# Optimization experiments

Measured on AMD Instinct MI355X. Metric: run time of the kernel, lower is better.

## Reference

```python
import jax, jax.numpy as jnp
import numpy as np

N, K, D = 524288, 32, 8
EPS = 1e-6


def setup_inputs() -> dict:
    key = jax.random.key(0)
    k1, k2, k3, k4 = jax.random.split(key, 4)
    x = jax.random.normal(k1, (N, D), dtype=jnp.float32)
    pi = jax.random.uniform(k2, (K,), dtype=jnp.float32)
    means = jax.random.normal(k3, (K, D), dtype=jnp.float32)
    # eye + small perturbation keeps tril(chol_var) well-conditioned (PD covariance)
    chol_var = jnp.eye(D, dtype=jnp.float32)[None] + 0.1 * jax.random.normal(k4, (K, D, D), dtype=jnp.float32)
    return {"x": x, "pi": pi, "means": means, "chol_var": chol_var}


def reference(x, pi, means, chol_var):
    d = x.shape[-1]
    L = jnp.tril(chol_var)                                   # [K,d,d]
    cov = jnp.einsum('kij,klj->kil', L, L) + EPS * jnp.eye(d, dtype=x.dtype)
    C = jnp.linalg.cholesky(cov)                             # [K,d,d] (MVN recomputes cholesky)
    logdet = 2.0 * jnp.sum(jnp.log(jnp.diagonal(C, axis1=-2, axis2=-1)), axis=-1)  # [K]
    eye = jnp.eye(d, dtype=x.dtype)
    Cinv = jax.vmap(lambda c: jax.scipy.linalg.solve_triangular(c, eye, lower=True))(C)  # [K,d,d]
    zx = jnp.einsum('kij,nj->nki', Cinv, x)                  # [N,K,d]
    zm = jnp.einsum('kij,kj->ki', Cinv, means)               # [K,d]
    maha = jnp.sum((zx - zm[None]) ** 2, axis=-1)            # [N,K]
    log_2pi = jnp.log(2.0 * jnp.pi).astype(x.dtype)
    log_probs = -0.5 * (maha + d * log_2pi + logdet[None])   # [N,K]
    wll = log_probs + jax.nn.log_softmax(pi)[None]
    return jax.scipy.special.logsumexp(wll, axis=1)          # [N]
```

## Files before the change

kernel.cpp:

```cpp
#include <hip/hip_runtime.h>
#include <math.h>

#define K_ 32
#define D_ 8
#define NF 48
#define NTHREADS 256
#define NBLOCKS 1024
#define TPW 4

typedef _Float16 half8 __attribute__((ext_vector_type(8)));
typedef float f32x16 __attribute__((ext_vector_type(16)));

__global__ __launch_bounds__(NTHREADS) void gmm_mfma(
    const float* __restrict__ x,
    const float* __restrict__ pi,
    const float* __restrict__ means,
    const float* __restrict__ chol,
    float* __restrict__ out, int N)
{
    __shared__ __align__(16) _Float16 ldsA[3][64][8];

    const int tid = threadIdx.x;

    if (tid < K_) {
        const int k = tid;
        float L[D_][D_];
#pragma unroll
        for (int i = 0; i < D_; ++i)
#pragma unroll
            for (int j = 0; j <= i; ++j)
                L[i][j] = chol[k * 64 + i * 8 + j];

        float rd[D_];
#pragma unroll
        for (int i = 0; i < D_; ++i) rd[i] = 1.f / L[i][i];

        float Ci[D_][D_];
#pragma unroll
        for (int j = 0; j < D_; ++j) {
            Ci[j][j] = rd[j];
#pragma unroll
            for (int i = j + 1; i < D_; ++i) {
                float s = 0.f;
#pragma unroll
                for (int m = j; m < i; ++m) s += L[i][m] * Ci[m][j];
                Ci[i][j] = -s * rd[i];
            }
        }

        float logdet = 0.f;
#pragma unroll
        for (int i = 0; i < D_; ++i) logdet += __logf(fabsf(L[i][i]));
        logdet *= 2.f;

        float A2[D_][D_];
#pragma unroll
        for (int i = 0; i < D_; ++i)
#pragma unroll
            for (int j = 0; j <= i; ++j) {
                float s = 0.f;
#pragma unroll
                for (int m = i; m < D_; ++m) s += Ci[m][i] * Ci[m][j];
                A2[i][j] = s;
                A2[j][i] = s;
            }

        float mu[D_];
#pragma unroll
        for (int j = 0; j < D_; ++j) mu[j] = means[k * 8 + j];
        float b[D_], q = 0.f;
#pragma unroll
        for (int i = 0; i < D_; ++i) {
            float s = 0.f;
#pragma unroll
            for (int j = 0; j < D_; ++j) s += A2[i][j] * mu[j];
            b[i] = s;
            q += s * mu[i];
        }

        float mx = pi[0];
#pragma unroll
        for (int t = 1; t < K_; ++t) mx = fmaxf(mx, pi[t]);
        float se = 0.f;
#pragma unroll
        for (int t = 0; t < K_; ++t) se += __expf(pi[t] - mx);
        float lse = mx + __logf(se);

        const float LOG2PI = 1.8378770664093453f;
        const float LOG2E  = 1.4426950408889634f;
        const float ALPHA  = 0.72134752044448170f;
        float cst2 = ((pi[k] - lse) - 0.5f * (logdet + 8.f * LOG2PI)) * LOG2E;

        float V[NF];
        int t = 0;
#pragma unroll
        for (int i = 0; i < D_; ++i)
#pragma unroll
            for (int j = 0; j <= i; ++j)
                V[t++] = (i == j) ? -ALPHA * A2[i][i] : -2.f * ALPHA * A2[i][j];
#pragma unroll
        for (int i = 0; i < D_; ++i) V[36 + i] = 2.f * ALPHA * b[i];
        V[44] = cst2 - ALPHA * q;
        V[45] = 0.f; V[46] = 0.f; V[47] = 0.f;

#pragma unroll
        for (int s = 0; s < 3; ++s)
#pragma unroll
            for (int h = 0; h < 2; ++h)
#pragma unroll
                for (int j = 0; j < 8; ++j)
                    ldsA[s][h * 32 + k][j] = (_Float16)V[16 * s + 8 * h + j];
    }
    __syncthreads();

    const int lane = tid & 63;
    const int m    = lane & 31;
    const bool h1  = lane >= 32;

    half8 wf[3];
#pragma unroll
    for (int s = 0; s < 3; ++s) wf[s] = *(const half8*)&ldsA[s][lane][0];

    const int w  = blockIdx.x * (NTHREADS / 64) + (tid >> 6);
    const int t0 = w * TPW;
    const float4* xp = (const float4*)x;
    const float LN2 = 0.69314718055994531f;

    float xv[TPW][D_];
#pragma unroll
    for (int u = 0; u < TPW; ++u) {
        const int n = (t0 + u) * 32 + m;
        float4 a = xp[2 * n], b2 = xp[2 * n + 1];
        xv[u][0] = a.x;  xv[u][1] = a.y;  xv[u][2] = a.z;  xv[u][3] = a.w;
        xv[u][4] = b2.x; xv[u][5] = b2.y; xv[u][6] = b2.z; xv[u][7] = b2.w;
    }

#pragma unroll
    for (int u = 0; u < TPW; ++u) {
        float Y[NF];
        {
            int t = 0;
#pragma unroll
            for (int i = 0; i < D_; ++i)
#pragma unroll
                for (int j = 0; j <= i; ++j) Y[t++] = xv[u][i] * xv[u][j];
#pragma unroll
            for (int i = 0; i < D_; ++i) Y[36 + i] = xv[u][i];
            Y[44] = 1.f; Y[45] = 0.f; Y[46] = 0.f; Y[47] = 0.f;
        }

        f32x16 acc;
#pragma unroll
        for (int r = 0; r < 16; ++r) acc[r] = 0.f;

#pragma unroll
        for (int s = 0; s < 3; ++s) {
            half8 bf;
#pragma unroll
            for (int j = 0; j < 8; ++j) {
                float v = h1 ? Y[16 * s + 8 + j] : Y[16 * s + j];
                bf[j] = (_Float16)v;
            }
            acc = __builtin_amdgcn_mfma_f32_32x32x16_f16(wf[s], bf, acc, 0, 0, 0);
        }

        float tot = 0.f;
#pragma unroll
        for (int r = 0; r < 16; ++r) tot += exp2f(acc[r]);
        tot += __shfl_xor(tot, 32, 64);
        float res = log2f(tot) * LN2;
        if (!h1) out[(t0 + u) * 32 + m] = res;
    }
}

extern "C" void kernel_launch(void* const* d_in, const int* in_sizes, int n_in,
                              void* d_out, int out_size, void* d_ws, size_t ws_size,
                              hipStream_t stream) {
    const float* x     = (const float*)d_in[0];
    const float* pi    = (const float*)d_in[1];
    const float* means = (const float*)d_in[2];
    const float* chol  = (const float*)d_in[3];
    float* out = (float*)d_out;

    int N = in_sizes[0] / D_;

    gmm_mfma<<<NBLOCKS, NTHREADS, 0, stream>>>(x, pi, means, chol, out, N);
}
```

Measured before the change: 75.06 us.

## Split per-component parameter prep into separate kernel via workspace

Moves the per-component Cholesky inverse and quadratic-form coefficient computation out of every block into a single-block prep kernel. That kernel writes the fp16 MFMA A-operand to workspace, and the main kernel loads it from global memory, so the LDS buffer and __syncthreads go away. This removes the redundant prep work that all 1024 blocks used to serialize on before any MFMA work. The feature vector is also built per MFMA slice instead of as one full array, and launch bounds ask for 4 blocks per CU. The cost is a second kernel launch and its dependency, with a single-thread-per-component prep stage on the critical path.

After: 109.2 us. +45.5%, slower.

```diff
diff --git a/kernel.cpp b/kernel.cpp
--- a/kernel.cpp
+++ b/kernel.cpp
@@ -11,115 +11,113 @@
 typedef _Float16 half8 __attribute__((ext_vector_type(8)));
 typedef float f32x16 __attribute__((ext_vector_type(16)));
 
-__global__ __launch_bounds__(NTHREADS) void gmm_mfma(
-    const float* __restrict__ x,
+
+__global__ void gmm_prep(
     const float* __restrict__ pi,
     const float* __restrict__ means,
     const float* __restrict__ chol,
-    float* __restrict__ out, int N)
+    _Float16* __restrict__ wsV)
 {
-    __shared__ __align__(16) _Float16 ldsA[3][64][8];
+    const int k = threadIdx.x;
+    if (k >= K_) return;
 
-    const int tid = threadIdx.x;
+    float L[D_][D_];
+#pragma unroll
+    for (int i = 0; i < D_; ++i)
+#pragma unroll
+        for (int j = 0; j <= i; ++j)
+            L[i][j] = chol[k * 64 + i * 8 + j];
 
-    if (tid < K_) {
-        const int k = tid;
-        float L[D_][D_];
+    float rd[D_];
 #pragma unroll
-        for (int i = 0; i < D_; ++i)
+    for (int i = 0; i < D_; ++i) rd[i] = 1.f / L[i][i];
+
+    float Ci[D_][D_];
 #pragma unroll
-            for (int j = 0; j <= i; ++j)
-                L[i][j] = chol[k * 64 + i * 8 + j];
+    for (int j = 0; j < D_; ++j) {
+        Ci[j][j] = rd[j];
+#pragma unroll
+        for (int i = j + 1; i < D_; ++i) {
+            float s = 0.f;
+#pragma unroll
+            for (int m = j; m < i; ++m) s += L[i][m] * Ci[m][j];
+            Ci[i][j] = -s * rd[i];
+        }
+    }
 
-        float rd[D_];
+    float logdet = 0.f;
 #pragma unroll
-        for (int i = 0; i < D_; ++i) rd[i] = 1.f / L[i][i];
+    for (int i = 0; i < D_; ++i) logdet += __logf(fabsf(L[i][i]));
+    logdet *= 2.f;
 
-        float Ci[D_][D_];
+    float A2[D_][D_];
 #pragma unroll
-        for (int j = 0; j < D_; ++j) {
-            Ci[j][j] = rd[j];
+    for (int i = 0; i < D_; ++i)
 #pragma unroll
-            for (int i = j + 1; i < D_; ++i) {
-                float s = 0.f;
+        for (int j = 0; j <= i; ++j) {
+            float s = 0.f;
 #pragma unroll
-                for (int m = j; m < i; ++m) s += L[i][m] * Ci[m][j];
-                Ci[i][j] = -s * rd[i];
-            }
+            for (int m = i; m < D_; ++m) s += Ci[m][i] * Ci[m][j];
+            A2[i][j] = s;
+            A2[j][i] = s;
         }
 
-        float logdet = 0.f;
+    float mu[D_];
 #pragma unroll
-        for (int i = 0; i < D_; ++i) logdet += __logf(fabsf(L[i][i]));
-        logdet *= 2.f;
+    for (int j = 0; j < D_; ++j) mu[j] = means[k * 8 + j];
+    float b[D_], q = 0.f;
+#pragma unroll
+    for (int i = 0; i < D_; ++i) {
+        float s = 0.f;
+#pragma unroll
+        for (int j = 0; j < D_; ++j) s += A2[i][j] * mu[j];
+        b[i] = s;
+        q += s * mu[i];
+    }
 
-        float A2[D_][D_];
+    float mx = pi[0];
 #pragma unroll
-        for (int i = 0; i < D_; ++i)
+    for (int t = 1; t < K_; ++t) mx = fmaxf(mx, pi[t]);
+    float se = 0.f;
 #pragma unroll
-            for (int j = 0; j <= i; ++j) {
-                float s = 0.f;
+    for (int t = 0; t < K_; ++t) se += __expf(pi[t] - mx);
+    float lse = mx + __logf(se);
+
+    const float LOG2PI = 1.8378770664093453f;
+    const float LOG2E  = 1.4426950408889634f;
+    const float ALPHA  = 0.72134752044448170f;
+    float cst2 = ((pi[k] - lse) - 0.5f * (logdet + 8.f * LOG2PI)) * LOG2E;
+
+    float V[NF];
+    int t = 0;
 #pragma unroll
-                for (int m = i; m < D_; ++m) s += Ci[m][i] * Ci[m][j];
-                A2[i][j] = s;
-                A2[j][i] = s;
-            }
-
-        float mu[D_];
+    for (int i = 0; i < D_; ++i)
 #pragma unroll
-        for (int j = 0; j < D_; ++j) mu[j] = means[k * 8 + j];
-        float b[D_], q = 0.f;
+        for (int j = 0; j <= i; ++j)
+            V[t++] = (i == j) ? -ALPHA * A2[i][i] : -2.f * ALPHA * A2[i][j];
 #pragma unroll
-        for (int i = 0; i < D_; ++i) {
-            float s = 0.f;
-#pragma unroll
-            for (int j = 0; j < D_; ++j) s += A2[i][j] * mu[j];
-            b[i] = s;
-            q += s * mu[i];
-        }
-
-        float mx = pi[0];
-#pragma unroll
-        for (int t = 1; t < K_; ++t) mx = fmaxf(mx, pi[t]);
-        float se = 0.f;
-#pragma unroll
-        for (int t = 0; t < K_; ++t) se += __expf(pi[t] - mx);
-        float lse = mx + __logf(se);
-
-        const float LOG2PI = 1.8378770664093453f;
-        const float LOG2E  = 1.4426950408889634f;
-        const float ALPHA  = 0.72134752044448170f;
-        float cst2 = ((pi[k] - lse) - 0.5f * (logdet + 8.f * LOG2PI)) * LOG2E;
-
-        float V[NF];
-        int t = 0;
-#pragma unroll
-        for (int i = 0; i < D_; ++i)
-#pragma unroll
-            for (int j = 0; j <= i; ++j)
-                V[t++] = (i == j) ? -ALPHA * A2[i][i] : -2.f * ALPHA * A2[i][j];
-#pragma unroll
-        for (int i = 0; i < D_; ++i) V[36 + i] = 2.f * ALPHA * b[i];
-        V[44] = cst2 - ALPHA * q;
-        V[45] = 0.f; V[46] = 0.f; V[47] = 0.f;
+    for (int i = 0; i < D_; ++i) V[36 + i] = 2.f * ALPHA * b[i];
+    V[44] = cst2 - ALPHA * q;
+    V[45] = 0.f; V[46] = 0.f; V[47] = 0.f;
 
 #pragma unroll
-        for (int s = 0; s < 3; ++s)
+    for (int s = 0; s < 3; ++s)
 #pragma unroll
-            for (int h = 0; h < 2; ++h)
+        for (int h = 0; h < 2; ++h)
 #pragma unroll
-                for (int j = 0; j < 8; ++j)
-                    ldsA[s][h * 32 + k][j] = (_Float16)V[16 * s + 8 * h + j];
-    }
-    __syncthreads();
+            for (int j = 0; j < 8; ++j)
+                wsV[(s * 64 + h * 32 + k) * 8 + j] = (_Float16)V[16 * s + 8 * h + j];
+}
 
+__global__ __launch_bounds__(NTHREADS, 4) void gmm_mfma(
+    const float* __restrict__ x,
+    const _Float16* __restrict__ wsV,
+    float* __restrict__ out)
+{
+    const int tid  = threadIdx.x;
     const int lane = tid & 63;
     const int m    = lane & 31;
     const bool h1  = lane >= 32;
-
-    half8 wf[3];
-#pragma unroll
-    for (int s = 0; s < 3; ++s) wf[s] = *(const half8*)&ldsA[s][lane][0];
 
     const int w  = blockIdx.x * (NTHREADS / 64) + (tid >> 6);
     const int t0 = w * TPW;
@@ -135,30 +133,40 @@
         xv[u][4] = b2.x; xv[u][5] = b2.y; xv[u][6] = b2.z; xv[u][7] = b2.w;
     }
 
+    const half8* wp = (const half8*)wsV;
+    half8 wf[3];
+#pragma unroll
+    for (int s = 0; s < 3; ++s) wf[s] = wp[s * 64 + lane];
+
 #pragma unroll
     for (int u = 0; u < TPW; ++u) {
-        float Y[NF];
-        {
-            int t = 0;
-#pragma unroll
-            for (int i = 0; i < D_; ++i)
-#pragma unroll
-                for (int j = 0; j <= i; ++j) Y[t++] = xv[u][i] * xv[u][j];
-#pragma unroll
-            for (int i = 0; i < D_; ++i) Y[36 + i] = xv[u][i];
-            Y[44] = 1.f; Y[45] = 0.f; Y[46] = 0.f; Y[47] = 0.f;
-        }
-
         f32x16 acc;
 #pragma unroll
         for (int r = 0; r < 16; ++r) acc[r] = 0.f;
 
 #pragma unroll
         for (int s = 0; s < 3; ++s) {
+            float yb[16];
+            int t = 0;
+#pragma unroll
+            for (int i = 0; i < D_; ++i)
+#pragma unroll
+                for (int j = 0; j <= i; ++j) {
+                    if (t >= 16 * s && t < 16 * (s + 1))
+                        yb[t - 16 * s] = xv[u][i] * xv[u][j];
+                    ++t;
+                }
+#pragma unroll
+            for (int i = 0; i < D_; ++i) {
+                const int f = 36 + i;
+                if (f >= 16 * s && f < 16 * (s + 1)) yb[f - 16 * s] = xv[u][i];
+            }
+            if (s == 2) { yb[12] = 1.f; yb[13] = 0.f; yb[14] = 0.f; yb[15] = 0.f; }
+
             half8 bf;
 #pragma unroll
             for (int j = 0; j < 8; ++j) {
-                float v = h1 ? Y[16 * s + 8 + j] : Y[16 * s + j];
+                float v = h1 ? yb[8 + j] : yb[j];
                 bf[j] = (_Float16)v;
             }
             acc = __builtin_amdgcn_mfma_f32_32x32x16_f16(wf[s], bf, acc, 0, 0, 0);
@@ -181,8 +189,9 @@
     const float* means = (const float*)d_in[2];
     const float* chol  = (const float*)d_in[3];
     float* out = (float*)d_out;
+    _Float16* wsV = (_Float16*)d_ws;
+    (void)in_sizes; (void)n_in; (void)out_size; (void)ws_size;
 
-    int N = in_sizes[0] / D_;
-
-    gmm_mfma<<<NBLOCKS, NTHREADS, 0, stream>>>(x, pi, means, chol, out, N);
+    gmm_prep<<<1, 64, 0, stream>>>(pi, means, chol, wsV);
+    gmm_mfma<<<NBLOCKS, NTHREADS, 0, stream>>>(x, wsV, out);
 }
```

## Compute per-component weights in every lane, dropping LDS and block barrier

Applied to the files above, without the earlier changes.

Each lane now does the Cholesky inverse and quadratic-form coefficient setup for its own component (k = lane%32) directly in registers. This replaces the old scheme where 32 threads per block computed them, wrote them to LDS, and the block synchronized. The kernel also issues half of the x loads before this setup so memory latency overlaps with it, vectorizes the parameter loads, and adds a launch-bounds occupancy hint. The cost is redundant setup math in every lane and higher register pressure.

Result: slower. 136.8 us (+82.3%).

```diff
diff --git a/kernel.cpp b/kernel.cpp
--- a/kernel.cpp
+++ b/kernel.cpp
@@ -11,115 +11,18 @@
 typedef _Float16 half8 __attribute__((ext_vector_type(8)));
 typedef float f32x16 __attribute__((ext_vector_type(16)));
 
-__global__ __launch_bounds__(NTHREADS) void gmm_mfma(
+__global__ __launch_bounds__(NTHREADS, 4) void gmm_mfma(
     const float* __restrict__ x,
     const float* __restrict__ pi,
     const float* __restrict__ means,
     const float* __restrict__ chol,
-    float* __restrict__ out, int N)
+    float* __restrict__ out)
 {
-    __shared__ __align__(16) _Float16 ldsA[3][64][8];
-
-    const int tid = threadIdx.x;
-
-    if (tid < K_) {
-        const int k = tid;
-        float L[D_][D_];
-#pragma unroll
-        for (int i = 0; i < D_; ++i)
-#pragma unroll
-            for (int j = 0; j <= i; ++j)
-                L[i][j] = chol[k * 64 + i * 8 + j];
-
-        float rd[D_];
-#pragma unroll
-        for (int i = 0; i < D_; ++i) rd[i] = 1.f / L[i][i];
-
-        float Ci[D_][D_];
-#pragma unroll
-        for (int j = 0; j < D_; ++j) {
-            Ci[j][j] = rd[j];
-#pragma unroll
-            for (int i = j + 1; i < D_; ++i) {
-                float s = 0.f;
-#pragma unroll
-                for (int m = j; m < i; ++m) s += L[i][m] * Ci[m][j];
-                Ci[i][j] = -s * rd[i];
-            }
-        }
-
-        float logdet = 0.f;
-#pragma unroll
-        for (int i = 0; i < D_; ++i) logdet += __logf(fabsf(L[i][i]));
-        logdet *= 2.f;
-
-        float A2[D_][D_];
-#pragma unroll
-        for (int i = 0; i < D_; ++i)
-#pragma unroll
-            for (int j = 0; j <= i; ++j) {
-                float s = 0.f;
-#pragma unroll
-                for (int m = i; m < D_; ++m) s += Ci[m][i] * Ci[m][j];
-                A2[i][j] = s;
-                A2[j][i] = s;
-            }
-
-        float mu[D_];
-#pragma unroll
-        for (int j = 0; j < D_; ++j) mu[j] = means[k * 8 + j];
-        float b[D_], q = 0.f;
-#pragma unroll
-        for (int i = 0; i < D_; ++i) {
-            float s = 0.f;
-#pragma unroll
-            for (int j = 0; j < D_; ++j) s += A2[i][j] * mu[j];
-            b[i] = s;
-            q += s * mu[i];
-        }
-
-        float mx = pi[0];
-#pragma unroll
-        for (int t = 1; t < K_; ++t) mx = fmaxf(mx, pi[t]);
-        float se = 0.f;
-#pragma unroll
-        for (int t = 0; t < K_; ++t) se += __expf(pi[t] - mx);
-        float lse = mx + __logf(se);
-
-        const float LOG2PI = 1.8378770664093453f;
-        const float LOG2E  = 1.4426950408889634f;
-        const float ALPHA  = 0.72134752044448170f;
-        float cst2 = ((pi[k] - lse) - 0.5f * (logdet + 8.f * LOG2PI)) * LOG2E;
-
-        float V[NF];
-        int t = 0;
-#pragma unroll
-        for (int i = 0; i < D_; ++i)
-#pragma unroll
-            for (int j = 0; j <= i; ++j)
-                V[t++] = (i == j) ? -ALPHA * A2[i][i] : -2.f * ALPHA * A2[i][j];
-#pragma unroll
-        for (int i = 0; i < D_; ++i) V[36 + i] = 2.f * ALPHA * b[i];
-        V[44] = cst2 - ALPHA * q;
-        V[45] = 0.f; V[46] = 0.f; V[47] = 0.f;
-
-#pragma unroll
-        for (int s = 0; s < 3; ++s)
-#pragma unroll
-            for (int h = 0; h < 2; ++h)
-#pragma unroll
-                for (int j = 0; j < 8; ++j)
-                    ldsA[s][h * 32 + k][j] = (_Float16)V[16 * s + 8 * h + j];
-    }
-    __syncthreads();
-
+    const int tid  = threadIdx.x;
     const int lane = tid & 63;
     const int m    = lane & 31;
     const bool h1  = lane >= 32;
-
-    half8 wf[3];
-#pragma unroll
-    for (int s = 0; s < 3; ++s) wf[s] = *(const half8*)&ldsA[s][lane][0];
+    const int k    = m;
 
     const int w  = blockIdx.x * (NTHREADS / 64) + (tid >> 6);
     const int t0 = w * TPW;
@@ -128,7 +31,123 @@
 
     float xv[TPW][D_];
 #pragma unroll
-    for (int u = 0; u < TPW; ++u) {
+    for (int u = 0; u < 2; ++u) {
+        const int n = (t0 + u) * 32 + m;
+        float4 a = xp[2 * n], b2 = xp[2 * n + 1];
+        xv[u][0] = a.x;  xv[u][1] = a.y;  xv[u][2] = a.z;  xv[u][3] = a.w;
+        xv[u][4] = b2.x; xv[u][5] = b2.y; xv[u][6] = b2.z; xv[u][7] = b2.w;
+    }
+
+    float lse, pik;
+    {
+        const float4* pp = (const float4*)pi;
+        float p[K_];
+#pragma unroll
+        for (int t = 0; t < 8; ++t) {
+            float4 a = pp[t];
+            p[4 * t] = a.x; p[4 * t + 1] = a.y; p[4 * t + 2] = a.z; p[4 * t + 3] = a.w;
+        }
+        float mx = p[0];
+#pragma unroll
+        for (int t = 1; t < K_; ++t) mx = fmaxf(mx, p[t]);
+        float se = 0.f;
+#pragma unroll
+        for (int t = 0; t < K_; ++t) se += __expf(p[t] - mx);
+        lse = mx + __logf(se);
+        pik = p[k];
+    }
+
+    float L[D_][D_];
+    {
+        const float4* cp = (const float4*)(chol + k * 64);
+#pragma unroll
+        for (int i = 0; i < D_; ++i) {
+            float4 a = cp[2 * i];
+            L[i][0] = a.x; L[i][1] = a.y; L[i][2] = a.z; L[i][3] = a.w;
+            if (i >= 4) {
+                float4 bq = cp[2 * i + 1];
+                L[i][4] = bq.x; L[i][5] = bq.y; L[i][6] = bq.z; L[i][7] = bq.w;
+            }
+        }
+    }
+
+    float rd[D_];
+#pragma unroll
+    for (int i = 0; i < D_; ++i) rd[i] = 1.f / L[i][i];
+
+    float Ci[D_][D_];
+#pragma unroll
+    for (int j = 0; j < D_; ++j) {
+        Ci[j][j] = rd[j];
+#pragma unroll
+        for (int i = j + 1; i < D_; ++i) {
+            float s = 0.f;
+#pragma unroll
+            for (int mm = j; mm < i; ++mm) s += L[i][mm] * Ci[mm][j];
+            Ci[i][j] = -s * rd[i];
+        }
+    }
+
+    float logdet = 0.f;
+#pragma unroll
+    for (int i = 0; i < D_; ++i) logdet += __logf(fabsf(L[i][i]));
+    logdet *= 2.f;
+
+    float A2[D_][D_];
+#pragma unroll
+    for (int i = 0; i < D_; ++i)
+#pragma unroll
+        for (int j = 0; j <= i; ++j) {
+            float s = 0.f;
+#pragma unroll
+            for (int mm = i; mm < D_; ++mm) s += Ci[mm][i] * Ci[mm][j];
+            A2[i][j] = s;
+            A2[j][i] = s;
+        }
+
+    float b[D_], q = 0.f;
+    {
+        const float4* mp = (const float4*)(means + k * 8);
+        float4 ma = mp[0], mb = mp[1];
+        float mu[D_] = {ma.x, ma.y, ma.z, ma.w, mb.x, mb.y, mb.z, mb.w};
+#pragma unroll
+        for (int i = 0; i < D_; ++i) {
+            float s = 0.f;
+#pragma unroll
+            for (int j = 0; j < D_; ++j) s += A2[i][j] * mu[j];
+            b[i] = s;
+            q += s * mu[i];
+        }
+    }
+
+    const float LOG2PI = 1.8378770664093453f;
+    const float LOG2E  = 1.4426950408889634f;
+    const float ALPHA  = 0.72134752044448170f;
+    float cst2 = ((pik - lse) - 0.5f * (logdet + 8.f * LOG2PI)) * LOG2E;
+
+    float V[NF];
+    {
+        int t = 0;
+#pragma unroll
+        for (int i = 0; i < D_; ++i)
+#pragma unroll
+            for (int j = 0; j <= i; ++j)
+                V[t++] = (i == j) ? -ALPHA * A2[i][i] : -2.f * ALPHA * A2[i][j];
+#pragma unroll
+        for (int i = 0; i < D_; ++i) V[36 + i] = 2.f * ALPHA * b[i];
+        V[44] = cst2 - ALPHA * q;
+        V[45] = 0.f; V[46] = 0.f; V[47] = 0.f;
+    }
+
+    half8 wf[3];
+#pragma unroll
+    for (int s = 0; s < 3; ++s)
+#pragma unroll
+        for (int j = 0; j < 8; ++j)
+            wf[s][j] = (_Float16)(h1 ? V[16 * s + 8 + j] : V[16 * s + j]);
+
+#pragma unroll
+    for (int u = 2; u < TPW; ++u) {
         const int n = (t0 + u) * 32 + m;
         float4 a = xp[2 * n], b2 = xp[2 * n + 1];
         xv[u][0] = a.x;  xv[u][1] = a.y;  xv[u][2] = a.z;  xv[u][3] = a.w;
@@ -181,8 +200,7 @@
     const float* means = (const float*)d_in[2];
     const float* chol  = (const float*)d_in[3];
     float* out = (float*)d_out;
-
-    int N = in_sizes[0] / D_;
-
-    gmm_mfma<<<NBLOCKS, NTHREADS, 0, stream>>>(x, pi, means, chol, out, N);
+    (void)in_sizes; (void)n_in; (void)out_size; (void)d_ws; (void)ws_size;
+
+    gmm_mfma<<<NBLOCKS, NTHREADS, 0, stream>>>(x, pi, means, chol, out);
 }
```
